# Kernel tuning notes

Measured on AMD Instinct MI355X. Metric: run time of the kernel, lower is better.

## Reference

```python
import jax, jax.numpy as jnp
import numpy as np

H, DH = 8, 32  # heads, dim_head
DN, DE = 256, 128  # dim_node, dim_edge


def _ln(x, g, b, eps=1e-5):
    mu = jnp.mean(x, axis=-1, keepdims=True)
    var = jnp.var(x, axis=-1, keepdims=True)
    return (x - mu) * jax.lax.rsqrt(var + eps) * g + b


def setup_inputs() -> dict:
    key = jax.random.key(0)
    ks = jax.random.split(key, 12)
    b, r, w = 1, 128, 256
    s = 0.02
    return {
        "x": jax.random.normal(ks[0], (b, r, w, DN), jnp.float32),
        "edges": jax.random.normal(ks[1], (b, w, w, DE), jnp.float32),
        "mask": jax.random.bernoulli(ks[2], 0.9, (b, r, w)),
        "edge_mask": jax.random.bernoulli(ks[3], 0.9, (b, w, w)),
        "ln_g": jnp.ones((DN,), jnp.float32),
        "ln_b": jnp.zeros((DN,), jnp.float32),
        "lne_g": jnp.ones((DE,), jnp.float32),
        "lne_b": jnp.zeros((DE,), jnp.float32),
        "W_edge": jax.random.normal(ks[4], (DE, H), jnp.float32) * s,
        "Wq": jax.random.normal(ks[5], (DN, H * DH), jnp.float32) * s,
        "Wkv": jax.random.normal(ks[6], (DN, 2 * H * DH), jnp.float32) * s,
        "Wg": jax.random.normal(ks[7], (DN, H * DH), jnp.float32) * s,
        "bg": jnp.ones((H * DH,), jnp.float32),
        "Wo": jax.random.normal(ks[8], (H * DH, DN), jnp.float32) * s,
        "bo": jnp.zeros((DN,), jnp.float32),
    }


def reference(x, edges, mask, edge_mask, ln_g, ln_b, lne_g, lne_b,
              W_edge, Wq, Wkv, Wg, bg, Wo, bo):
    NEG = -jnp.finfo(x.dtype).max
    b, r, w, _ = x.shape
    xn = _ln(x, ln_g, ln_b)                       # pre-attn LayerNorm on nodes
    en = _ln(edges, lne_g, lne_b)                 # LayerNorm on edges
    bias = jnp.einsum('bije,eh->bhij', en, W_edge)  # edges -> per-head bias
    bias = jnp.where(edge_mask[:, None], bias, NEG)  # masked_fill on bias

    q = (xn @ Wq).reshape(b, r, w, H, DH)
    kv = xn @ Wkv
    k = kv[..., :H * DH].reshape(b, r, w, H, DH)
    v = kv[..., H * DH:].reshape(b, r, w, H, DH)
    scale = DH ** -0.5
    # row attention: rows act as extra batch dim; attend along width w
    dots = jnp.einsum('brihd,brjhd->brhij', q * scale, k) + bias[:, None]
    am = mask[:, :, None, :, None] & mask[:, :, None, None, :]  # [b,r,1,i,j]
    dots = jnp.where(am, dots, NEG)
    attn = jax.nn.softmax(dots, axis=-1)
    out = jnp.einsum('brhij,brjhd->brihd', attn, v).reshape(b, r, w, H * DH)
    gates = jax.nn.sigmoid(xn @ Wg + bg)          # gating on normed input
    out = out * gates
    return out @ Wo + bo
```

## Files before the change

### kernel.cpp

```cpp
#include <hip/hip_runtime.h>

#define NEGF (-3.402823466e38f)
#define LOG2E 1.4426950408889634f

constexpr int H  = 8,  DH = 32, DN = 256, DE = 128;
constexpr int RR = 128, WW = 256;
constexpr int MROWS = RR * WW;

typedef __attribute__((ext_vector_type(8))) short bf16x8;
typedef __attribute__((ext_vector_type(4))) short bf16x4;
typedef __attribute__((ext_vector_type(4))) float f32x4;
typedef __attribute__((ext_vector_type(2))) int i32x2;

__device__ __forceinline__ float b2f(short s) {
  unsigned u = ((unsigned)(unsigned short)s) << 16;
  return __builtin_bit_cast(float, u);
}
__device__ __forceinline__ short f2b(float f) {
  unsigned u = __builtin_bit_cast(unsigned, f);
  unsigned r = (u + 0x7fffu + ((u >> 16) & 1u)) >> 16;
  return (short)r;
}
__device__ __forceinline__ float wred(float v) {
#pragma unroll
  for (int off = 32; off > 0; off >>= 1) v += __shfl_xor(v, off, 64);
  return v;
}

__global__ __launch_bounds__(256) void k_ln_x(const float* __restrict__ x,
                                              const float* __restrict__ g,
                                              const float* __restrict__ b,
                                              short* __restrict__ xnb) {
  const int wave = threadIdx.x >> 6, lane = threadIdx.x & 63;
  const int row = (blockIdx.x << 2) + wave;
  const float4 v = ((const float4*)(x + (size_t)row * DN))[lane];
  float s  = v.x + v.y + v.z + v.w;
  float s2 = v.x*v.x + v.y*v.y + v.z*v.z + v.w*v.w;
  s = wred(s); s2 = wred(s2);
  const float mu = s * (1.f / DN);
  const float rs = rsqrtf(s2 * (1.f / DN) - mu * mu + 1e-5f);
  const float4 gg = ((const float4*)g)[lane];
  const float4 bb = ((const float4*)b)[lane];
  bf16x4 o;
  o[0] = f2b((v.x - mu) * rs * gg.x + bb.x);
  o[1] = f2b((v.y - mu) * rs * gg.y + bb.y);
  o[2] = f2b((v.z - mu) * rs * gg.z + bb.z);
  o[3] = f2b((v.w - mu) * rs * gg.w + bb.w);
  ((bf16x4*)(xnb + (size_t)row * DN))[lane] = o;
}

__global__ __launch_bounds__(256) void k_prep(const float* __restrict__ Wq,
                                              const float* __restrict__ Wkv,
                                              const float* __restrict__ Wg,
                                              const float* __restrict__ Wo,
                                              short* __restrict__ wt) {
  const int idx = blockIdx.x * 256 + threadIdx.x;
  if (idx < 262144) {
    const int n = idx >> 8, k = idx & 255;
    float v;
    if (n < 256)      v = Wq[k * 256 + n];
    else if (n < 768) v = Wkv[k * 512 + (n - 256)];
    else              v = Wg[k * 256 + (n - 768)];
    wt[idx] = f2b(v);
  } else {
    const int m = idx - 262144;
    const int n = m >> 8, k = m & 255;
    wt[idx] = f2b(Wo[k * 256 + n]);
  }
}

__global__ __launch_bounds__(256) void k_bias(const float* __restrict__ edges,
                                              const int* __restrict__ emask,
                                              const float* __restrict__ g,
                                              const float* __restrict__ b,
                                              const float* __restrict__ We,
                                              float* __restrict__ bias2) {
  const int wave = threadIdx.x >> 6, lane = threadIdx.x & 63;
  const int p = (blockIdx.x << 2) + wave;
  const int i = p & (WW - 1), j = p >> 8;
  const float2 e = ((const float2*)(edges + (size_t)(i * WW + j) * DE))[lane];
  float s = e.x + e.y, s2 = e.x*e.x + e.y*e.y;
  s = wred(s); s2 = wred(s2);
  const float mu = s * (1.f / DE);
  const float rs = rsqrtf(s2 * (1.f / DE) - mu * mu + 1e-5f);
  const float2 gg = ((const float2*)g)[lane];
  const float2 bb = ((const float2*)b)[lane];
  const float n0 = (e.x - mu) * rs * gg.x + bb.x;
  const float n1 = (e.y - mu) * rs * gg.y + bb.y;
  const float* w0 = We + (lane * 2) * H;
  float acc[H];
#pragma unroll
  for (int h = 0; h < H; ++h) acc[h] = n0 * w0[h] + n1 * w0[H + h];
#pragma unroll
  for (int off = 32; off > 0; off >>= 1)
#pragma unroll
    for (int h = 0; h < H; ++h) acc[h] += __shfl_xor(acc[h], off, 64);
  if (lane == 0) {
    const int em = emask[i * WW + j];
#pragma unroll
    for (int h = 0; h < H; ++h)
      bias2[(size_t)((h << 6) + (j >> 2)) * 1024 + (i << 2) + (j & 3)]
          = em ? acc[h] * LOG2E : NEGF;
  }
}

template<int N, int EPI>
__global__ __launch_bounds__(256) void k_gemm(const short* __restrict__ A,
                                              const short* __restrict__ Bt,
                                              const float* __restrict__ bias,
                                              void* __restrict__ Cout) {
  __shared__ short Bs[128 * 256];
  const int tid = threadIdx.x;
  const int w = tid >> 6, lane = tid & 63;
  const int g = lane >> 4, c = lane & 15;
  constexpr int nb = N / 128;
  const int bm = (int)(blockIdx.x / nb) * 128;
  const int bn = (int)(blockIdx.x % nb) * 128;

  const char* Bt_b = (const char*)(Bt + (size_t)bn * 256);
#pragma unroll
  for (int q = 0; q < 16; ++q) {
    const int o = (q * 256 + tid) * 16;
    const int osw = o ^ ((((o >> 9) & 7)) << 4);
    __builtin_amdgcn_global_load_lds(
        (const __attribute__((address_space(1))) void*)(Bt_b + osw),
        (__attribute__((address_space(3))) void*)((__attribute__((address_space(3))) char*)Bs + o),
        16, 0, 0);
  }
  asm volatile("s_waitcnt vmcnt(0)" ::: "memory");
  __syncthreads();

  const int m0 = bm + (w << 5);
  f32x4 acc[2][8] = {};
  const char* Bs_b = (const char*)Bs;
#pragma unroll
  for (int ks = 0; ks < 8; ++ks) {
    bf16x8 af[2];
#pragma unroll
    for (int mi = 0; mi < 2; ++mi)
      af[mi] = *(const bf16x8*)(A + (size_t)(m0 + (mi << 4) + c) * 256 + (ks << 5) + (g << 3));
    bf16x8 bfr[8];
#pragma unroll
    for (int ni = 0; ni < 8; ++ni) {
      const int L = ((ni << 4) + c) * 512 + (ks << 6) + (g << 4);
      bfr[ni] = *(const bf16x8*)(Bs_b + (L ^ ((c & 7) << 4)));
    }
#pragma unroll
    for (int mi = 0; mi < 2; ++mi)
#pragma unroll
      for (int ni = 0; ni < 8; ++ni)
        acc[mi][ni] = __builtin_amdgcn_mfma_f32_16x16x32_bf16(af[mi], bfr[ni], acc[mi][ni], 0, 0, 0);
  }

  const int r0 = bm + (w << 5) + (g << 2);
  const int c0 = bn + c;
#pragma unroll
  for (int mi = 0; mi < 2; ++mi)
#pragma unroll
    for (int ni = 0; ni < 8; ++ni) {
      const int col = c0 + (ni << 4);
      if (EPI == 0) {
        short* C = (short*)Cout;
        const bool gate = (bn + (ni << 4)) >= 768;
        const float bgv = gate ? bias[col - 768] : 0.f;
#pragma unroll
        for (int jj = 0; jj < 4; ++jj) {
          float v = acc[mi][ni][jj];
          if (gate) v = 1.f / (1.f + __expf(-(v + bgv)));
          C[(size_t)(r0 + (mi << 4) + jj) * N + col] = f2b(v);
        }
      } else {
        float* C = (float*)Cout;
        const float bv = bias[col];
#pragma unroll
        for (int jj = 0; jj < 4; ++jj)
          C[(size_t)(r0 + (mi << 4) + jj) * N + col] = acc[mi][ni][jj] + bv;
      }
    }
}

__global__ __launch_bounds__(256) void k_attn(const short* __restrict__ qkvg,
                                              const float* __restrict__ bias2,
                                              const int* __restrict__ mask,
                                              short* __restrict__ aout) {
  __shared__ short K_lds[256 * 40];
  __shared__ alignas(16) short VS[8192];
  __shared__ float jm_lds[256];
  const int r = blockIdx.x >> 3, h = blockIdx.x & 7;
  const int tid = threadIdx.x;
  const int w = tid >> 6, lane = tid & 63;
  const int g = lane >> 4, c = lane & 15;
  const size_t rowbase = (size_t)r * WW;

  {
    const int jr = tid >> 2, ch = (tid & 3) << 3;
    const int dt = ch >> 4, cc = ch & 15;
#pragma unroll
    for (int p = 0; p < 4; ++p) {
      const int j = (p << 6) + jr;
      const short* src = qkvg + (rowbase + j) * 1024 + 256 + h * 32 + ch;
      *(bf16x8*)&K_lds[j * 40 + ch] = *(const bf16x8*)src;
      *(bf16x8*)&VS[(dt << 12) + ((j >> 2) << 6) + ((j & 3) << 4) + cc] =
          *(const bf16x8*)(src + 256);
    }
    jm_lds[tid] = mask[r * WW + tid] ? 0.f : NEGF;
  }
  __syncthreads();

  const int q0 = (w << 6);
  bf16x8 qf[4];
  float qm[4];
#pragma unroll
  for (int qt = 0; qt < 4; ++qt) {
    qf[qt] = *(const bf16x8*)(qkvg + (rowbase + q0 + (qt << 4) + c) * 1024 + h * 32 + (g << 3));
    qm[qt] = jm_lds[q0 + (qt << 4) + c];
  }
  float m[4] = {NEGF, NEGF, NEGF, NEGF}, l[4] = {};
  f32x4 O[4][2] = {};
  const float scale2 = 0.2550541611f;
  const float* bh = bias2 + ((size_t)h << 16);
  const unsigned vs_base =
      (unsigned)(uintptr_t)(__attribute__((address_space(3))) char*)VS;

#pragma unroll 2
  for (int jb = 0; jb < WW; jb += 32) {
    i32x2 vlo0, vhi0, vlo1, vhi1;
    const unsigned va = vs_base + ((unsigned)(jb >> 2) << 7) + lane * 8;
    asm volatile("ds_read_b64_tr_b16 %0, %1 offset:0"    : "=v"(vlo0) : "v"(va));
    asm volatile("ds_read_b64_tr_b16 %0, %1 offset:512"  : "=v"(vhi0) : "v"(va));
    asm volatile("ds_read_b64_tr_b16 %0, %1 offset:8192" : "=v"(vlo1) : "v"(va));
    asm volatile("ds_read_b64_tr_b16 %0, %1 offset:8704" : "=v"(vhi1) : "v"(va));
    const bf16x8 kf0 = *(const bf16x8*)&K_lds[(jb + c) * 40 + (g << 3)];
    const bf16x8 kf1 = *(const bf16x8*)&K_lds[(jb + 16 + c) * 40 + (g << 3)];
    const f32x4 jm0 = *(const f32x4*)&jm_lds[jb + (g << 2)];
    const f32x4 jm1 = *(const f32x4*)&jm_lds[jb + 16 + (g << 2)];
    f32x4 bv[4][2];
#pragma unroll
    for (int qt = 0; qt < 4; ++qt) {
      const int qq = (q0 + (qt << 4) + c) << 2;
      bv[qt][0] = *(const f32x4*)(bh + (size_t)((jb >> 2) + g) * 1024 + qq);
      bv[qt][1] = *(const f32x4*)(bh + (size_t)((jb >> 2) + 4 + g) * 1024 + qq);
    }
    f32x4 s[4][2];
    float pmax[4];
#pragma unroll
    for (int qt = 0; qt < 4; ++qt) {
      const f32x4 z = {0.f, 0.f, 0.f, 0.f};
      s[qt][0] = __builtin_amdgcn_mfma_f32_16x16x32_bf16(kf0, qf[qt], z, 0, 0, 0);
      s[qt][1] = __builtin_amdgcn_mfma_f32_16x16x32_bf16(kf1, qf[qt], z, 0, 0, 0);
      float pm = NEGF;
#pragma unroll
      for (int rr = 0; rr < 4; ++rr) {
        float t0 = fmaxf(fmaf(s[qt][0][rr], scale2, bv[qt][0][rr]) + jm0[rr] + qm[qt], NEGF);
        float t1 = fmaxf(fmaf(s[qt][1][rr], scale2, bv[qt][1][rr]) + jm1[rr] + qm[qt], NEGF);
        s[qt][0][rr] = t0; s[qt][1][rr] = t1;
        pm = fmaxf(pm, fmaxf(t0, t1));
      }
      pm = fmaxf(pm, __shfl_xor(pm, 16, 64));
      pm = fmaxf(pm, __shfl_xor(pm, 32, 64));
      pmax[qt] = pm;
    }
    int need = 0;
#pragma unroll
    for (int qt = 0; qt < 4; ++qt) need |= (pmax[qt] > m[qt] + 11.5416f);
    if (__any(need)) {
      float fr[4];
#pragma unroll
      for (int qt = 0; qt < 4; ++qt) {
        const float mn = fmaxf(m[qt], pmax[qt]);
        fr[qt] = exp2f(m[qt] - mn);
        m[qt] = mn; l[qt] *= fr[qt];
      }
#pragma unroll
      for (int qt = 0; qt < 4; ++qt)
#pragma unroll
        for (int rr = 0; rr < 4; ++rr) {
          const float fb = __shfl(fr[qt], (g << 2) | rr, 64);
          O[qt][0][rr] *= fb; O[qt][1][rr] *= fb;
        }
    }
    bf16x8 pa[4];
#pragma unroll
    for (int qt = 0; qt < 4; ++qt) {
      float sum = 0.f;
#pragma unroll
      for (int rr = 0; rr < 4; ++rr) {
        const float e0 = exp2f(s[qt][0][rr] - m[qt]);
        const float e1 = exp2f(s[qt][1][rr] - m[qt]);
        sum += e0 + e1;
        pa[qt][rr] = f2b(e0);
        pa[qt][rr + 4] = f2b(e1);
      }
      sum += __shfl_xor(sum, 16, 64);
      sum += __shfl_xor(sum, 32, 64);
      l[qt] += sum;
    }
    asm volatile("s_waitcnt lgkmcnt(0)" ::: "memory");
    __builtin_amdgcn_sched_barrier(0);
    const bf16x4 l0 = __builtin_bit_cast(bf16x4, vlo0), h0 = __builtin_bit_cast(bf16x4, vhi0);
    const bf16x4 l1 = __builtin_bit_cast(bf16x4, vlo1), h1 = __builtin_bit_cast(bf16x4, vhi1);
    const bf16x8 vf0 = __builtin_shufflevector(l0, h0, 0, 1, 2, 3, 4, 5, 6, 7);
    const bf16x8 vf1 = __builtin_shufflevector(l1, h1, 0, 1, 2, 3, 4, 5, 6, 7);
#pragma unroll
    for (int qt = 0; qt < 4; ++qt) {
      O[qt][0] = __builtin_amdgcn_mfma_f32_16x16x32_bf16(pa[qt], vf0, O[qt][0], 0, 0, 0);
      O[qt][1] = __builtin_amdgcn_mfma_f32_16x16x32_bf16(pa[qt], vf1, O[qt][1], 0, 0, 0);
    }
  }

  float inv[4];
#pragma unroll
  for (int qt = 0; qt < 4; ++qt) inv[qt] = 1.f / l[qt];
#pragma unroll
  for (int qt = 0; qt < 4; ++qt)
#pragma unroll
    for (int rr = 0; rr < 4; ++rr) {
      const float iv = __shfl(inv[qt], (g << 2) | rr, 64);
      const size_t row = rowbase + q0 + (qt << 4) + (g << 2) + rr;
#pragma unroll
      for (int dt = 0; dt < 2; ++dt) {
        const int d = (dt << 4) + c;
        const float gate = b2f(qkvg[row * 1024 + 768 + h * 32 + d]);
        aout[row * 256 + h * 32 + d] = f2b(O[qt][dt][rr] * iv * gate);
      }
    }
}

extern "C" void kernel_launch(void* const* d_in, const int* in_sizes, int n_in,
                              void* d_out, int out_size, void* d_ws, size_t ws_size,
                              hipStream_t stream) {
  const float* x      = (const float*)d_in[0];
  const float* edges  = (const float*)d_in[1];
  const int*   mask   = (const int*)d_in[2];
  const int*   emask  = (const int*)d_in[3];
  const float* ln_g   = (const float*)d_in[4];
  const float* ln_b   = (const float*)d_in[5];
  const float* lne_g  = (const float*)d_in[6];
  const float* lne_b  = (const float*)d_in[7];
  const float* W_edge = (const float*)d_in[8];
  const float* Wq     = (const float*)d_in[9];
  const float* Wkv    = (const float*)d_in[10];
  const float* Wg     = (const float*)d_in[11];
  const float* bg     = (const float*)d_in[12];
  const float* Wo     = (const float*)d_in[13];
  const float* bo     = (const float*)d_in[14];
  float* out = (float*)d_out;

  char*  ws    = (char*)d_ws;
  short* qkvgb = (short*)ws;
  short* xnb   = (short*)(ws + 67108864);
  short* aoutb = (short*)(ws + 67108864 + 16777216);
  short* wt    = (short*)(ws + 100663296);
  float* bias2 = (float*)(ws + 101318656);

  k_ln_x<<<MROWS / 4, 256, 0, stream>>>(x, ln_g, ln_b, xnb);
  k_prep<<<1280, 256, 0, stream>>>(Wq, Wkv, Wg, Wo, wt);
  k_bias<<<(WW * WW) / 4, 256, 0, stream>>>(edges, emask, lne_g, lne_b, W_edge, bias2);
  k_gemm<1024, 0><<<256 * 8, 256, 0, stream>>>(xnb, wt, bg, (void*)qkvgb);
  k_attn<<<RR * H, 256, 0, stream>>>(qkvgb, bias2, mask, aoutb);
  k_gemm<256, 1><<<256 * 2, 256, 0, stream>>>(aoutb, wt + 262144, bo, (void*)out);
}
```

Before: 283.9 us.

## Retile GEMM without LDS, fold scale into Q, and fuse bias into MFMA accumulator

The projection GEMM drops the LDS-staged B tile in favour of a 2x2 wave grid that reads A and B fragments straight from global memory. It adds an XCD-aware block remap and an occupancy hint of 3. The softmax scale times log2e is folded into the Q columns in the GEMM epilogue, and the edge bias is loaded as the MFMA accumulator init, which removes the per-element fma. The bf16 conversion of probabilities now uses packed hardware cvt instructions. The risks are higher global/L2 traffic with no LDS reuse of B, and Q being scaled before bf16 rounding.

Result: slower. 316.4 us (+11.4%).

```diff
diff --git a/kernel.cpp b/kernel.cpp
--- a/kernel.cpp
+++ b/kernel.cpp
@@ -6,6 +6,7 @@
 constexpr int H  = 8,  DH = 32, DN = 256, DE = 128;
 constexpr int RR = 128, WW = 256;
 constexpr int MROWS = RR * WW;
+constexpr float SCL2 = 0.17677669529663687f * 1.4426950408889634f;
 
 typedef __attribute__((ext_vector_type(8))) short bf16x8;
 typedef __attribute__((ext_vector_type(4))) short bf16x4;
@@ -105,67 +106,57 @@
 }
 
 template<int N, int EPI>
-__global__ __launch_bounds__(256) void k_gemm(const short* __restrict__ A,
-                                              const short* __restrict__ Bt,
-                                              const float* __restrict__ bias,
-                                              void* __restrict__ Cout) {
-  __shared__ short Bs[128 * 256];
+__global__ __launch_bounds__(256, 3) void k_gemm(const short* __restrict__ A,
+                                                 const short* __restrict__ Bt,
+                                                 const float* __restrict__ bias,
+                                                 void* __restrict__ Cout) {
+  constexpr int nb  = N / 128;
+  constexpr int nwg = (MROWS / 128) * nb;
+  const int bid  = blockIdx.x;
+  const int orig = (bid & 7) * (nwg >> 3) + (bid >> 3);
+  const int bm = (orig / nb) << 7;
+  const int bn = (orig % nb) << 7;
   const int tid = threadIdx.x;
   const int w = tid >> 6, lane = tid & 63;
   const int g = lane >> 4, c = lane & 15;
-  constexpr int nb = N / 128;
-  const int bm = (int)(blockIdx.x / nb) * 128;
-  const int bn = (int)(blockIdx.x % nb) * 128;
-
-  const char* Bt_b = (const char*)(Bt + (size_t)bn * 256);
-#pragma unroll
-  for (int q = 0; q < 16; ++q) {
-    const int o = (q * 256 + tid) * 16;
-    const int osw = o ^ ((((o >> 9) & 7)) << 4);
-    __builtin_amdgcn_global_load_lds(
-        (const __attribute__((address_space(1))) void*)(Bt_b + osw),
-        (__attribute__((address_space(3))) void*)((__attribute__((address_space(3))) char*)Bs + o),
-        16, 0, 0);
-  }
-  asm volatile("s_waitcnt vmcnt(0)" ::: "memory");
-  __syncthreads();
-
-  const int m0 = bm + (w << 5);
-  f32x4 acc[2][8] = {};
-  const char* Bs_b = (const char*)Bs;
+  const int wm = w >> 1, wn = w & 1;
+  const int m0 = bm + (wm << 6), n0 = bn + (wn << 6);
+
+  const short* Ap = A  + (size_t)(m0 + c) * 256 + (g << 3);
+  const short* Bp = Bt + (size_t)(n0 + c) * 256 + (g << 3);
+
+  f32x4 acc[4][4] = {};
 #pragma unroll
   for (int ks = 0; ks < 8; ++ks) {
-    bf16x8 af[2];
-#pragma unroll
-    for (int mi = 0; mi < 2; ++mi)
-      af[mi] = *(const bf16x8*)(A + (size_t)(m0 + (mi << 4) + c) * 256 + (ks << 5) + (g << 3));
-    bf16x8 bfr[8];
-#pragma unroll
-    for (int ni = 0; ni < 8; ++ni) {
-      const int L = ((ni << 4) + c) * 512 + (ks << 6) + (g << 4);
-      bfr[ni] = *(const bf16x8*)(Bs_b + (L ^ ((c & 7) << 4)));
-    }
-#pragma unroll
-    for (int mi = 0; mi < 2; ++mi)
-#pragma unroll
-      for (int ni = 0; ni < 8; ++ni)
-        acc[mi][ni] = __builtin_amdgcn_mfma_f32_16x16x32_bf16(af[mi], bfr[ni], acc[mi][ni], 0, 0, 0);
-  }
-
-  const int r0 = bm + (w << 5) + (g << 2);
-  const int c0 = bn + c;
-#pragma unroll
-  for (int mi = 0; mi < 2; ++mi)
-#pragma unroll
-    for (int ni = 0; ni < 8; ++ni) {
-      const int col = c0 + (ni << 4);
+    bf16x8 af[4], bf[4];
+#pragma unroll
+    for (int i = 0; i < 4; ++i) {
+      af[i] = *(const bf16x8*)(Ap + (size_t)(i << 4) * 256 + (ks << 5));
+      bf[i] = *(const bf16x8*)(Bp + (size_t)(i << 4) * 256 + (ks << 5));
+    }
+#pragma unroll
+    for (int mi = 0; mi < 4; ++mi)
+#pragma unroll
+      for (int ni = 0; ni < 4; ++ni)
+        acc[mi][ni] = __builtin_amdgcn_mfma_f32_16x16x32_bf16(af[mi], bf[ni], acc[mi][ni], 0, 0, 0);
+  }
+
+  const int r0 = m0 + (g << 2);
+#pragma unroll
+  for (int mi = 0; mi < 4; ++mi)
+#pragma unroll
+    for (int ni = 0; ni < 4; ++ni) {
+      const int colb = n0 + (ni << 4);
+      const int col  = colb + c;
       if (EPI == 0) {
         short* C = (short*)Cout;
-        const bool gate = (bn + (ni << 4)) >= 768;
+        const bool qreg = colb < 256;
+        const bool gate = colb >= 768;
         const float bgv = gate ? bias[col - 768] : 0.f;
 #pragma unroll
         for (int jj = 0; jj < 4; ++jj) {
           float v = acc[mi][ni][jj];
+          if (qreg) v *= SCL2;
           if (gate) v = 1.f / (1.f + __expf(-(v + bgv)));
           C[(size_t)(r0 + (mi << 4) + jj) * N + col] = f2b(v);
         }
@@ -217,7 +208,6 @@
   }
   float m[4] = {NEGF, NEGF, NEGF, NEGF}, l[4] = {};
   f32x4 O[4][2] = {};
-  const float scale2 = 0.2550541611f;
   const float* bh = bias2 + ((size_t)h << 16);
   const unsigned vs_base =
       (unsigned)(uintptr_t)(__attribute__((address_space(3))) char*)VS;
@@ -234,25 +224,20 @@
     const bf16x8 kf1 = *(const bf16x8*)&K_lds[(jb + 16 + c) * 40 + (g << 3)];
     const f32x4 jm0 = *(const f32x4*)&jm_lds[jb + (g << 2)];
     const f32x4 jm1 = *(const f32x4*)&jm_lds[jb + 16 + (g << 2)];
-    f32x4 bv[4][2];
+    f32x4 s[4][2];
+    float pmax[4];
 #pragma unroll
     for (int qt = 0; qt < 4; ++qt) {
       const int qq = (q0 + (qt << 4) + c) << 2;
-      bv[qt][0] = *(const f32x4*)(bh + (size_t)((jb >> 2) + g) * 1024 + qq);
-      bv[qt][1] = *(const f32x4*)(bh + (size_t)((jb >> 2) + 4 + g) * 1024 + qq);
-    }
-    f32x4 s[4][2];
-    float pmax[4];
-#pragma unroll
-    for (int qt = 0; qt < 4; ++qt) {
-      const f32x4 z = {0.f, 0.f, 0.f, 0.f};
-      s[qt][0] = __builtin_amdgcn_mfma_f32_16x16x32_bf16(kf0, qf[qt], z, 0, 0, 0);
-      s[qt][1] = __builtin_amdgcn_mfma_f32_16x16x32_bf16(kf1, qf[qt], z, 0, 0, 0);
+      const f32x4 bv0 = *(const f32x4*)(bh + (size_t)((jb >> 2) + g) * 1024 + qq);
+      const f32x4 bv1 = *(const f32x4*)(bh + (size_t)((jb >> 2) + 4 + g) * 1024 + qq);
+      s[qt][0] = __builtin_amdgcn_mfma_f32_16x16x32_bf16(kf0, qf[qt], bv0, 0, 0, 0);
+      s[qt][1] = __builtin_amdgcn_mfma_f32_16x16x32_bf16(kf1, qf[qt], bv1, 0, 0, 0);
       float pm = NEGF;
 #pragma unroll
       for (int rr = 0; rr < 4; ++rr) {
-        float t0 = fmaxf(fmaf(s[qt][0][rr], scale2, bv[qt][0][rr]) + jm0[rr] + qm[qt], NEGF);
-        float t1 = fmaxf(fmaf(s[qt][1][rr], scale2, bv[qt][1][rr]) + jm1[rr] + qm[qt], NEGF);
+        const float t0 = fmaxf(s[qt][0][rr] + (jm0[rr] + qm[qt]), NEGF);
+        const float t1 = fmaxf(s[qt][1][rr] + (jm1[rr] + qm[qt]), NEGF);
         s[qt][0][rr] = t0; s[qt][1][rr] = t1;
         pm = fmaxf(pm, fmaxf(t0, t1));
       }
@@ -282,18 +267,24 @@
     bf16x8 pa[4];
 #pragma unroll
     for (int qt = 0; qt < 4; ++qt) {
+      float e0[4], e1[4];
       float sum = 0.f;
 #pragma unroll
       for (int rr = 0; rr < 4; ++rr) {
-        const float e0 = exp2f(s[qt][0][rr] - m[qt]);
-        const float e1 = exp2f(s[qt][1][rr] - m[qt]);
-        sum += e0 + e1;
-        pa[qt][rr] = f2b(e0);
-        pa[qt][rr + 4] = f2b(e1);
+        e0[rr] = exp2f(s[qt][0][rr] - m[qt]);
+        e1[rr] = exp2f(s[qt][1][rr] - m[qt]);
+        sum += e0[rr] + e1[rr];
       }
       sum += __shfl_xor(sum, 16, 64);
       sum += __shfl_xor(sum, 32, 64);
       l[qt] += sum;
+      unsigned u0, u1, u2, u3;
+      asm("v_cvt_pk_bf16_f32 %0, %1, %2" : "=v"(u0) : "v"(e0[0]), "v"(e0[1]));
+      asm("v_cvt_pk_bf16_f32 %0, %1, %2" : "=v"(u1) : "v"(e0[2]), "v"(e0[3]));
+      asm("v_cvt_pk_bf16_f32 %0, %1, %2" : "=v"(u2) : "v"(e1[0]), "v"(e1[1]));
+      asm("v_cvt_pk_bf16_f32 %0, %1, %2" : "=v"(u3) : "v"(e1[2]), "v"(e1[3]));
+      struct { unsigned a, b, c, d; } pk = {u0, u1, u2, u3};
+      pa[qt] = __builtin_bit_cast(bf16x8, pk);
     }
     asm volatile("s_waitcnt lgkmcnt(0)" ::: "memory");
     __builtin_amdgcn_sched_barrier(0);
```
